# Optimization experiments

Hardware: AMD Instinct MI355X
Metric: run time of the kernel (lower is better)

Reference implementation:

```python
import jax, jax.numpy as jnp
import numpy as np

D = 1024      # d_model
H = 16        # nhead
DH = D // H   # d_head = 64
DC = D // 4   # d_compress = 256
HID = 2048    # dim_feedforward (SwiGLU hidden)
G = 2         # num_groups
EPG = 4       # experts_per_gp
E = G * EPG   # num_experts = 8
TOPK = 2
EPS = 1e-6
B, T = 2, 2048


def _rope_sincos(t, dh):
    inv_freq = 1.0 / (10000.0 ** (jnp.arange(0, dh, 2, dtype=jnp.float32) / dh))
    ang = jnp.arange(t, dtype=jnp.float32)[:, None] * inv_freq[None, :]  # [T, dh/2]
    return jnp.sin(ang), jnp.cos(ang)


def _apply_rope(x, sin, cos):
    # x: [B, H, T, DH]; sin/cos: [T, DH/2] broadcast over B,H
    x1 = x[..., ::2]
    x2 = x[..., 1::2]
    r = jnp.stack([x1 * cos - x2 * sin, x1 * sin + x2 * cos], axis=-1)
    return r.reshape(x.shape)


def _swiglu(x):
    a, b = jnp.split(x, 2, axis=-1)
    return jax.nn.silu(a) * b


def _rmsnorm(x, w):
    return x * jax.lax.rsqrt(jnp.mean(x * x, axis=-1, keepdims=True) + EPS) * w


def reference(src, Wq, Wk_c, Wv_c, Wk, Wv, Wo,
              W_shared_in, W_shared_out, W1_shared, W2_experts,
              Wg_gate, We_gate, group_bias, expert_bias, norm1_w, norm2_w):
    Bb, Tt, C = src.shape
    # ---- Latent attention (K/V compressed to d_c then re-expanded) ----
    q = (src @ Wq).reshape(Bb, Tt, H, DH).transpose(0, 2, 1, 3)
    k = ((src @ Wk_c) @ Wk).reshape(Bb, Tt, H, DH).transpose(0, 2, 1, 3)
    v = ((src @ Wv_c) @ Wv).reshape(Bb, Tt, H, DH).transpose(0, 2, 1, 3)
    sin, cos = _rope_sincos(Tt, DH)
    q = _apply_rope(q, sin, cos)
    k = _apply_rope(k, sin, cos)
    attn = jnp.einsum('bhqd,bhkd->bhqk', q, k) / np.sqrt(DH).astype(np.float32)
    attn = jax.nn.softmax(attn, axis=-1)
    sa = jnp.einsum('bhqk,bhkd->bhqd', attn, v)
    sa = sa.transpose(0, 2, 1, 3).reshape(Bb, Tt, C) @ Wo
    x = _rmsnorm(src + sa, norm1_w)

    # ---- Hierarchical MoE FFN ----
    S = Bb * Tt
    flat = x.reshape(S, C)
    shared = _swiglu(flat @ W_shared_in) @ W_shared_out          # [S, C]
    g_probs = jax.nn.softmax(flat @ Wg_gate + group_bias, -1)    # [S, G]
    g_idx = jnp.argmax(g_probs, axis=-1)                          # [S]
    e_logits = flat @ We_gate + expert_bias                       # [S, E]
    e_group = jnp.arange(E) // EPG
    in_group = e_group[None, :] == g_idx[:, None]                 # [S, E]
    e_probs = jax.nn.softmax(jnp.where(in_group, e_logits, -jnp.inf), -1)
    g_prob = jnp.take_along_axis(g_probs, g_idx[:, None], axis=1)  # [S, 1]
    p_expert = e_probs * g_prob
    topv, topi = jax.lax.top_k(p_expert, TOPK)                    # [S, K]
    # dense combine weights: zero for non-selected experts (same math as dispatch loop)
    w = jnp.zeros((S, E), flat.dtype).at[jnp.arange(S)[:, None], topi].set(topv)
    h = _swiglu(flat @ W1_shared)                                 # [S, HID] (w1 shared by all experts)
    routed = jnp.zeros_like(shared)
    for e in range(E):  # fixed small expert count
        routed = routed + (h @ W2_experts[e]) * w[:, e:e + 1]
    out = x + (shared + routed).reshape(Bb, Tt, C)
    return _rmsnorm(out, norm2_w)


def setup_inputs() -> dict:
    key = jax.random.key(0)
    ks = jax.random.split(key, 14)
    s = 0.02
    return {
        'src': jax.random.normal(ks[0], (B, T, D), jnp.float32),
        'Wq': jax.random.normal(ks[1], (D, D), jnp.float32) * s,
        'Wk_c': jax.random.normal(ks[2], (D, DC), jnp.float32) * s,
        'Wv_c': jax.random.normal(ks[3], (D, DC), jnp.float32) * s,
        'Wk': jax.random.normal(ks[4], (DC, D), jnp.float32) * s,
        'Wv': jax.random.normal(ks[5], (DC, D), jnp.float32) * s,
        'Wo': jax.random.normal(ks[6], (D, D), jnp.float32) * s,
        'W_shared_in': jax.random.normal(ks[7], (D, 2 * HID), jnp.float32) * s,
        'W_shared_out': jax.random.normal(ks[8], (HID, D), jnp.float32) * s,
        'W1_shared': jax.random.normal(ks[9], (D, 2 * HID), jnp.float32) * s,
        'W2_experts': jax.random.normal(ks[10], (E, HID, D), jnp.float32) * s,
        'Wg_gate': jax.random.normal(ks[11], (D, G), jnp.float32) * s,
        'We_gate': jax.random.normal(ks[12], (D, E), jnp.float32) * s,
        'group_bias': jnp.zeros((G,), jnp.float32),
        'expert_bias': jnp.zeros((E,), jnp.float32),
        'norm1_w': jnp.ones((D,), jnp.float32),
        'norm2_w': jnp.ones((D,), jnp.float32),
    }
```

## Files before the change

kernel.cpp:

```cpp
#include <hip/hip_runtime.h>
#include <math.h>

#define D_    1024
#define H_    16
#define DH_   64
#define DC_   256
#define HID_  2048
#define E_    8
#define B_    2
#define T_    2048
#define S_    4096
#define EPS_  1e-6f
#define QKVW_ 3072

typedef unsigned short u16;
typedef short bf16x8 __attribute__((ext_vector_type(8)));
typedef float f32x4 __attribute__((ext_vector_type(4)));

__device__ __forceinline__ float b2f(u16 u) {
    return __uint_as_float(((unsigned int)u) << 16);
}
__device__ __forceinline__ u16 f2b(float f) {
    unsigned int u = __float_as_uint(f);
    u += 0x7FFF + ((u >> 16) & 1);
    return (u16)(u >> 16);
}
__device__ __forceinline__ void g2l16(const u16* g, u16* l) {
    __builtin_amdgcn_global_load_lds(
        (const __attribute__((address_space(1))) void*)g,
        (__attribute__((address_space(3))) void*)l, 16, 0, 0);
}

__global__ __launch_bounds__(256) void conv_t(const float* __restrict__ in,
                                              u16* __restrict__ out,
                                              int K, int N,
                                              long inZ, long outZ, int perm) {
    in  += (long)blockIdx.z * inZ;
    out += (long)blockIdx.z * outZ;
    __shared__ float t[32][33];
    const int n0 = blockIdx.x * 32, k0 = blockIdx.y * 32;
    int src_n0 = n0;
    if (perm) {
        int t64 = n0 >> 6;
        src_n0 = ((n0 & 63) == 0) ? t64 * 32 : (N / 2 + t64 * 32);
    }
    const int tx = threadIdx.x & 31, ty = threadIdx.x >> 5;
#pragma unroll
    for (int i = 0; i < 4; i++)
        t[ty + 8 * i][tx] = in[(long)(k0 + ty + 8 * i) * N + src_n0 + tx];
    __syncthreads();
#pragma unroll
    for (int i = 0; i < 4; i++)
        out[(long)(n0 + ty + 8 * i) * K + k0 + tx] = f2b(t[tx][ty + 8 * i]);
}

__global__ __launch_bounds__(256) void vt_conv(const u16* __restrict__ qkv,
                                               u16* __restrict__ vt) {
    __shared__ u16 t[32][34];
    const int bh = blockIdx.z;
    const int b = bh >> 4, h = bh & 15;
    const int t0 = blockIdx.x * 32, d0 = blockIdx.y * 32;
    const int tx = threadIdx.x & 31, ty = threadIdx.x >> 5;
#pragma unroll
    for (int i = 0; i < 4; i++)
        t[ty + 8 * i][tx] =
            qkv[((long)b * T_ + t0 + ty + 8 * i) * QKVW_ + 2048 + h * 64 + d0 + tx];
    __syncthreads();
#pragma unroll
    for (int i = 0; i < 4; i++)
        vt[((long)bh * 64 + d0 + ty + 8 * i) * T_ + t0 + tx] = t[tx][ty + 8 * i];
}

__global__ __launch_bounds__(256) void convert_bf16(const float* __restrict__ in,
                                                    u16* __restrict__ out, int n4) {
    int i = blockIdx.x * 256 + threadIdx.x;
    if (i >= n4) return;
    float4 f = ((const float4*)in)[i];
    ushort4 o;
    o.x = f2b(f.x); o.y = f2b(f.y); o.z = f2b(f.z); o.w = f2b(f.w);
    ((ushort4*)out)[i] = o;
}

template<int OUTMODE>
__global__ __launch_bounds__(256) void gemm_bf16(const u16* __restrict__ A,
                                                 const u16* __restrict__ Bt,
                                                 void* __restrict__ Cp,
                                                 int N, int K, int ldo,
                                                 void* __restrict__ Cp2) {
    __shared__ u16 As[128 * 32];
    __shared__ u16 Bs[128 * 32];
    const int tid  = threadIdx.x;
    const int lane = tid & 63;
    const int wv   = tid >> 6;
    const int wm   = wv >> 1, wn = wv & 1;
    const long row0 = (long)blockIdx.y * 128;
    const long col0 = (long)blockIdx.x * 128;
    const int Klocal = K / gridDim.z;
    const long koff  = (long)blockIdx.z * Klocal;

    f32x4 acc[4][4];
#pragma unroll
    for (int i = 0; i < 4; i++)
#pragma unroll
        for (int j = 0; j < 4; j++) acc[i][j] = (f32x4){0.f, 0.f, 0.f, 0.f};

    const int sr = tid >> 2;
    const int sc = (tid & 3) << 3;
    const u16* Ag  = A  + (row0 + sr) * (long)K + koff + sc;
    const u16* Ag2 = Ag + 64 * (long)K;
    const u16* Bg  = Bt + (col0 + sr) * (long)K + koff + sc;
    const u16* Bg2 = Bg + 64 * (long)K;
    u16* lA  = As + tid * 8;
    u16* lA2 = As + 2048 + tid * 8;
    u16* lB  = Bs + tid * 8;
    u16* lB2 = Bs + 2048 + tid * 8;

    const int fl = lane & 15;
    const int fk = (lane >> 4) << 3;
    const u16* ArA = As + (wm * 64 + fl) * 32 + fk;
    const u16* BrB = Bs + (wn * 64 + fl) * 32 + fk;

    for (int k0 = 0; k0 < Klocal; k0 += 32) {
        __syncthreads();
        g2l16(Ag + k0, lA);
        g2l16(Ag2 + k0, lA2);
        g2l16(Bg + k0, lB);
        g2l16(Bg2 + k0, lB2);
        __syncthreads();
        bf16x8 af[4], bfr[4];
#pragma unroll
        for (int mi = 0; mi < 4; mi++) af[mi]  = *(const bf16x8*)(ArA + mi * 512);
#pragma unroll
        for (int ni = 0; ni < 4; ni++) bfr[ni] = *(const bf16x8*)(BrB + ni * 512);
#pragma unroll
        for (int mi = 0; mi < 4; mi++)
#pragma unroll
            for (int ni = 0; ni < 4; ni++)
                acc[mi][ni] = __builtin_amdgcn_mfma_f32_16x16x32_bf16(
                    af[mi], bfr[ni], acc[mi][ni], 0, 0, 0);
    }

    const int cr = (lane >> 4) << 2;
    const int cc = lane & 15;
#pragma unroll
    for (int mi = 0; mi < 4; mi++) {
#pragma unroll
        for (int r = 0; r < 4; r++) {
            long grow = row0 + wm * 64 + mi * 16 + cr + r;
            if (OUTMODE == 3) {
                u16* outb = (u16*)Cp + (long)(blockIdx.x >> 5) * S_ * HID_;
                u16* hrow = outb + grow * ldo + (blockIdx.x & 31) * 64 + wn * 32;
#pragma unroll
                for (int ni = 0; ni < 2; ni++) {
                    float a = acc[mi][ni][r], b = acc[mi][ni + 2][r];
                    float sig = 1.f / (1.f + __expf(-a));
                    hrow[ni * 16 + cc] = f2b(a * sig * b);
                }
            } else {
#pragma unroll
                for (int ni = 0; ni < 4; ni++) {
                    long gcol = col0 + wn * 64 + ni * 16 + cc;
                    float v = acc[mi][ni][r];
                    if (OUTMODE == 1)      ((u16*)Cp)[grow * ldo + gcol] = f2b(v);
                    else if (OUTMODE == 2) ((u16*)Cp)[gcol * ldo + grow] = f2b(v);
                    else {
                        float* basep = (float*)(blockIdx.z ? Cp2 : Cp);
                        basep[grow * ldo + gcol] = v;
                    }
                }
            }
        }
    }
}

__global__ __launch_bounds__(256) void routed_gemm(const u16* __restrict__ Hh,
                                                   const u16* __restrict__ W2T,
                                                   const int* __restrict__ list,
                                                   const float* __restrict__ wlist,
                                                   const int* __restrict__ bases,
                                                   const int* __restrict__ counts,
                                                   float* __restrict__ Cout) {
    const int e    = blockIdx.y >> 5;
    const int tile = blockIdx.y & 31;
    const int cnt  = counts[e];
    if (tile * 128 >= cnt) return;
    const int base = bases[e];

    __shared__ u16 As[128 * 32];
    __shared__ u16 Bs[128 * 32];
    __shared__ int   toks[128];
    __shared__ float wrow[128];

    const int tid = threadIdx.x;
    if (tid < 128) {
        int ridx = tile * 128 + tid;
        if (ridx < cnt) { toks[tid] = list[base + ridx]; wrow[tid] = wlist[base + ridx]; }
        else            { toks[tid] = -1;                wrow[tid] = 0.f; }
    }
    __syncthreads();

    const int lane = tid & 63;
    const int wv   = tid >> 6;
    const int wm   = wv >> 1, wn = wv & 1;
    const long col0 = (long)blockIdx.x * 128;

    f32x4 acc[4][4];
#pragma unroll
    for (int i = 0; i < 4; i++)
#pragma unroll
        for (int j = 0; j < 4; j++) acc[i][j] = (f32x4){0.f, 0.f, 0.f, 0.f};

    const int sr = tid >> 2;
    const int sc = (tid & 3) << 3;
    const int t1 = toks[sr], t2 = toks[sr + 64];
    const u16* Ag  = Hh + (long)(t1 < 0 ? 0 : t1) * HID_ + sc;
    const u16* Ag2 = Hh + (long)(t2 < 0 ? 0 : t2) * HID_ + sc;
    const u16* Bg  = W2T + (long)e * D_ * HID_ + (col0 + sr) * (long)HID_ + sc;
    const u16* Bg2 = Bg + 64 * (long)HID_;
    u16* lA  = As + tid * 8;
    u16* lA2 = As + 2048 + tid * 8;
    u16* lB  = Bs + tid * 8;
    u16* lB2 = Bs + 2048 + tid * 8;

    const int fl = lane & 15;
    const int fk = (lane >> 4) << 3;
    const u16* ArA = As + (wm * 64 + fl) * 32 + fk;
    const u16* BrB = Bs + (wn * 64 + fl) * 32 + fk;

    for (int k0 = 0; k0 < HID_; k0 += 32) {
        __syncthreads();
        g2l16(Ag + k0, lA);
        g2l16(Ag2 + k0, lA2);
        g2l16(Bg + k0, lB);
        g2l16(Bg2 + k0, lB2);
        __syncthreads();
        bf16x8 af[4], bfr[4];
#pragma unroll
        for (int mi = 0; mi < 4; mi++) af[mi]  = *(const bf16x8*)(ArA + mi * 512);
#pragma unroll
        for (int ni = 0; ni < 4; ni++) bfr[ni] = *(const bf16x8*)(BrB + ni * 512);
#pragma unroll
        for (int mi = 0; mi < 4; mi++)
#pragma unroll
            for (int ni = 0; ni < 4; ni++)
                acc[mi][ni] = __builtin_amdgcn_mfma_f32_16x16x32_bf16(
                    af[mi], bfr[ni], acc[mi][ni], 0, 0, 0);
    }

    const int cr = (lane >> 4) << 2;
    const int cc = lane & 15;
#pragma unroll
    for (int mi = 0; mi < 4; mi++) {
#pragma unroll
        for (int r = 0; r < 4; r++) {
            int rr = wm * 64 + mi * 16 + cr + r;
            int tk = toks[rr];
            if (tk < 0) continue;
            float wvw = wrow[rr];
            float* crow = Cout + (long)tk * D_ + col0 + wn * 64;
#pragma unroll
            for (int ni = 0; ni < 4; ni++)
                atomicAdd(crow + ni * 16 + cc, acc[mi][ni][r] * wvw);
        }
    }
}

__global__ __launch_bounds__(256) void rope_table(float2* __restrict__ tab) {
    int idx = blockIdx.x * 256 + threadIdx.x;
    int t = idx >> 5, i = idx & 31;
    float ang = (float)t * powf(10000.f, -(float)i / 32.f);
    float sn, cs;
    sincosf(ang, &sn, &cs);
    tab[idx] = make_float2(sn, cs);
}

__global__ __launch_bounds__(256) void rope_apply(u16* __restrict__ qkv,
                                                  const float2* __restrict__ tab) {
    long p = (long)blockIdx.x * 256 + threadIdx.x;
    int s  = (int)(p >> 8);
    int c8 = (int)(p & 255) << 3;
    int t  = s & (T_ - 1);
    const float2* tp = tab + t * 32 + ((c8 & 63) >> 1);
    u16* px = qkv + (long)s * QKVW_ + c8;
    bf16x8 v = *(const bf16x8*)px;
    bf16x8 o;
#pragma unroll
    for (int j = 0; j < 4; j++) {
        float x1 = b2f((u16)v[2 * j]), x2 = b2f((u16)v[2 * j + 1]);
        float2 sc = tp[j];
        o[2 * j]     = (short)f2b(x1 * sc.y - x2 * sc.x);
        o[2 * j + 1] = (short)f2b(x1 * sc.x + x2 * sc.y);
    }
    *(bf16x8*)px = o;
}

__global__ __launch_bounds__(512) void attn_kernel(const u16* __restrict__ qkv,
                                                   const u16* __restrict__ vtg,
                                                   u16* __restrict__ sab) {
    __shared__ u16 Ks[2][128 * 64];
    __shared__ u16 Ps[8][16 * 128];
    const int tid  = threadIdx.x;
    const int lane = tid & 63;
    const int w    = tid >> 6;
    const int flat = blockIdx.x + (blockIdx.y << 4);
    const int virt = ((flat & 7) << 6) | (flat >> 3);
    const int qt = virt & 15;
    const int bh = virt >> 4;
    const int b  = bh >> 4, h = bh & 15;
    const long tok0 = (long)b * T_ + qt * 128;
    const int fl = lane & 15;
    const int fq = lane >> 4;

    bf16x8 qf0, qf1;
    {
        const u16* qp = qkv + (tok0 + w * 16 + fl) * QKVW_ + h * 64 + fq * 8;
        qf0 = *(const bf16x8*)qp;
        qf1 = *(const bf16x8*)(qp + 32);
    }

    const u16* kb0 = qkv + ((long)b * T_) * QKVW_ + 1024 + h * 64;
    const u16* vb0 = vtg + ((long)bh * 64) * T_;

    float m_[4], l_[4];
    f32x4 oacc[4];
#pragma unroll
    for (int i = 0; i < 4; i++) {
        m_[i] = -1e30f; l_[i] = 0.f;
        oacc[i] = (f32x4){0.f, 0.f, 0.f, 0.f};
    }

    auto stageK = [&](int kt, int buf) {
#pragma unroll
        for (int ps = 0; ps < 2; ps++) {
            int i = tid + ps * 512;
            int row = i >> 3, gg = i & 7;
            g2l16(kb0 + (long)(kt * 128 + row) * QKVW_ + ((gg ^ (row & 7)) << 3),
                  Ks[buf] + i * 8);
        }
    };

    stageK(0, 0);
    int cur = 0;
    for (int kt = 0; kt < T_ / 128; kt++) {
        __syncthreads();
        if (kt + 1 < T_ / 128) stageK(kt + 1, cur ^ 1);
        const u16* kbase = Ks[cur];

        f32x4 sacc[8];
#pragma unroll
        for (int ni = 0; ni < 8; ni++) sacc[ni] = (f32x4){0.f, 0.f, 0.f, 0.f};
        __builtin_amdgcn_s_setprio(1);
#pragma unroll
        for (int ks = 0; ks < 2; ks++) {
            bf16x8 qq = ks ? qf1 : qf0;
#pragma unroll
            for (int ni = 0; ni < 8; ni++) {
                bf16x8 kf = *(const bf16x8*)(kbase + (ni * 16 + fl) * 64 +
                                             (((ks * 4 + fq) ^ (fl & 7)) << 3));
                sacc[ni] = __builtin_amdgcn_mfma_f32_16x16x32_bf16(qq, kf, sacc[ni], 0, 0, 0);
            }
        }
        __builtin_amdgcn_s_setprio(0);

        float rmax[4];
#pragma unroll
        for (int r = 0; r < 4; r++) {
            float mm = sacc[0][r];
#pragma unroll
            for (int ni = 1; ni < 8; ni++) mm = fmaxf(mm, sacc[ni][r]);
            rmax[r] = mm * 0.125f;
        }
#pragma unroll
        for (int off = 1; off < 16; off <<= 1)
#pragma unroll
            for (int r = 0; r < 4; r++) rmax[r] = fmaxf(rmax[r], __shfl_xor(rmax[r], off));
        float alpha[4], psum[4];
#pragma unroll
        for (int r = 0; r < 4; r++) {
            float nm = fmaxf(m_[r], rmax[r]);
            alpha[r] = __expf(m_[r] - nm);
            m_[r] = nm;
            psum[r] = 0.f;
        }
        u16* pst = Ps[w];
#pragma unroll
        for (int ni = 0; ni < 8; ni++) {
            int colg = ni * 2 + (fl >> 3);
            int cl   = fl & 7;
#pragma unroll
            for (int r = 0; r < 4; r++) {
                int row = fq * 4 + r;
                float p = __expf(sacc[ni][r] * 0.125f - m_[r]);
                psum[r] += p;
                pst[row * 128 + ((colg ^ (row & 15)) << 3) + cl] = f2b(p);
            }
        }
#pragma unroll
        for (int off = 1; off < 16; off <<= 1)
#pragma unroll
            for (int r = 0; r < 4; r++) psum[r] += __shfl_xor(psum[r], off);
#pragma unroll
        for (int r = 0; r < 4; r++) l_[r] = l_[r] * alpha[r] + psum[r];
#pragma unroll
        for (int ni = 0; ni < 4; ni++)
#pragma unroll
            for (int r = 0; r < 4; r++) oacc[ni][r] *= alpha[r];

        __builtin_amdgcn_s_setprio(1);
#pragma unroll
        for (int ks = 0; ks < 4; ks++) {
            bf16x8 pf = *(const bf16x8*)(pst + fl * 128 +
                                         (((ks * 4 + fq) ^ fl) << 3));
#pragma unroll
            for (int ni = 0; ni < 4; ni++) {
                const u16* vp = vb0 + (long)(ni * 16 + fl) * T_ + kt * 128 +
                                ((ks * 4 + fq) << 3);
                bf16x8 vf = *(const bf16x8*)vp;
                oacc[ni] = __builtin_amdgcn_mfma_f32_16x16x32_bf16(pf, vf, oacc[ni], 0, 0, 0);
            }
        }
        __builtin_amdgcn_s_setprio(0);
        cur ^= 1;
    }

#pragma unroll
    for (int r = 0; r < 4; r++) {
        float inv = 1.f / l_[r];
        u16* op = sab + (tok0 + w * 16 + fq * 4 + r) * D_ + h * 64 + fl;
#pragma unroll
        for (int ni = 0; ni < 4; ni++) op[ni * 16] = f2b(oacc[ni][r] * inv);
    }
}

template<int BF>
__global__ __launch_bounds__(256) void rmsnorm_res(const float* __restrict__ a,
                                                   const float* __restrict__ b,
                                                   const float* __restrict__ b2,
                                                   const float* __restrict__ w,
                                                   float* __restrict__ outf,
                                                   u16* __restrict__ outb) {
    const int s = blockIdx.x;
    const float* ar = a + (long)s * D_;
    const float* br = b + (long)s * D_;
    const float* cr2 = b2 + (long)s * D_;
    float y[4];
    float ss = 0.f;
#pragma unroll
    for (int kx = 0; kx < 4; kx++) {
        int j = threadIdx.x + kx * 256;
        y[kx] = ar[j] + br[j] + cr2[j];
        ss += y[kx] * y[kx];
    }
    __shared__ float red[4];
#pragma unroll
    for (int off = 32; off > 0; off >>= 1) ss += __shfl_down(ss, off);
    int lane = threadIdx.x & 63, wv = threadIdx.x >> 6;
    if (lane == 0) red[wv] = ss;
    __syncthreads();
    float tot = red[0] + red[1] + red[2] + red[3];
    float scl = rsqrtf(tot / (float)D_ + EPS_);
    float* orow = outf + (long)s * D_;
#pragma unroll
    for (int kx = 0; kx < 4; kx++) {
        int j = threadIdx.x + kx * 256;
        float v = y[kx] * scl * w[j];
        orow[j] = v;
        if (BF) outb[(long)s * D_ + j] = f2b(v);
    }
}

__global__ __launch_bounds__(256) void gate_kernel(const float* __restrict__ x,
                                                   const float* __restrict__ Wg,
                                                   const float* __restrict__ We,
                                                   const float* __restrict__ gb,
                                                   const float* __restrict__ eb,
                                                   int* __restrict__ tok_e,
                                                   float* __restrict__ tok_w) {
    const int wave = threadIdx.x >> 6;
    const int lane = threadIdx.x & 63;
    const int s = blockIdx.x * 4 + wave;
    const float* xr = x + (long)s * D_;
    float g0 = 0.f, g1 = 0.f;
    float ee[8];
#pragma unroll
    for (int e = 0; e < 8; e++) ee[e] = 0.f;
    for (int j = lane; j < D_; j += 64) {
        float xv = xr[j];
        g0 += xv * Wg[j * 2 + 0];
        g1 += xv * Wg[j * 2 + 1];
#pragma unroll
        for (int e = 0; e < 8; e++) ee[e] += xv * We[j * 8 + e];
    }
#pragma unroll
    for (int off = 32; off > 0; off >>= 1) {
        g0 += __shfl_down(g0, off);
        g1 += __shfl_down(g1, off);
#pragma unroll
        for (int e = 0; e < 8; e++) ee[e] += __shfl_down(ee[e], off);
    }
    if (lane == 0) {
        g0 += gb[0];
        g1 += gb[1];
        int gidx = (g1 > g0) ? 1 : 0;
        float gm = fmaxf(g0, g1);
        float p0 = expf(g0 - gm), p1 = expf(g1 - gm);
        float gprob = (gidx ? p1 : p0) / (p0 + p1);
        int base = gidx * 4;
        float pe[4];
        float em = -1e30f;
#pragma unroll
        for (int i = 0; i < 4; i++) {
            pe[i] = ee[base + i] + eb[base + i];
            em = fmaxf(em, pe[i]);
        }
        float sum = 0.f;
#pragma unroll
        for (int i = 0; i < 4; i++) { pe[i] = expf(pe[i] - em); sum += pe[i]; }
        float inv = gprob / sum;
#pragma unroll
        for (int i = 0; i < 4; i++) pe[i] *= inv;
        int i1 = 0;
        for (int i = 1; i < 4; i++) if (pe[i] > pe[i1]) i1 = i;
        int i2 = -1;
        for (int i = 0; i < 4; i++) {
            if (i == i1) continue;
            if (i2 < 0 || pe[i] > pe[i2]) i2 = i;
        }
        tok_e[s * 2 + 0] = base + i1;
        tok_e[s * 2 + 1] = base + i2;
        tok_w[s * 2 + 0] = pe[i1];
        tok_w[s * 2 + 1] = pe[i2];
    }
}

__global__ __launch_bounds__(256) void route_build(const int* __restrict__ tok_e,
                                                   const float* __restrict__ tok_w,
                                                   int* __restrict__ counts_g,
                                                   int* __restrict__ bases_g,
                                                   int* __restrict__ list,
                                                   float* __restrict__ wlist) {
    __shared__ int cnt[E_], bas[E_], cur[E_];
    const int tid = threadIdx.x;
    if (tid < E_) cnt[tid] = 0;
    __syncthreads();
    for (int i = tid; i < 2 * S_; i += 256) atomicAdd(&cnt[tok_e[i]], 1);
    __syncthreads();
    if (tid == 0) {
        int acc = 0;
        for (int e = 0; e < E_; e++) { bas[e] = acc; cur[e] = acc; acc += cnt[e]; }
    }
    __syncthreads();
    if (tid < E_) { counts_g[tid] = cnt[tid]; bases_g[tid] = bas[tid]; }
    for (int i = tid; i < 2 * S_; i += 256) {
        int e = tok_e[i];
        int p = atomicAdd(&cur[e], 1);
        list[p] = i >> 1;
        wlist[p] = tok_w[i];
    }
}

extern "C" void kernel_launch(void* const* d_in, const int* in_sizes, int n_in,
                              void* d_out, int out_size, void* d_ws, size_t ws_size,
                              hipStream_t stream) {
    const float* src  = (const float*)d_in[0];
    const float* Wq   = (const float*)d_in[1];
    const float* Wk_c = (const float*)d_in[2];
    const float* Wv_c = (const float*)d_in[3];
    const float* Wk   = (const float*)d_in[4];
    const float* Wv   = (const float*)d_in[5];
    const float* Wo   = (const float*)d_in[6];
    const float* Wsin = (const float*)d_in[7];
    const float* Wsout= (const float*)d_in[8];
    const float* W1   = (const float*)d_in[9];
    const float* W2   = (const float*)d_in[10];
    const float* Wg   = (const float*)d_in[11];
    const float* We   = (const float*)d_in[12];
    const float* gb   = (const float*)d_in[13];
    const float* eb   = (const float*)d_in[14];
    const float* n1w  = (const float*)d_in[15];
    const float* n2w  = (const float*)d_in[16];
    float* out = (float*)d_out;

    const size_t MB = 1u << 20;
    char* w8 = (char*)d_ws;
    u16*  qkv   = (u16*)(w8);
    u16*  vtg   = (u16*)(w8 + 24 * MB);
    float* oproj0 = (float*)(w8);
    float* oproj1 = (float*)(w8 + 16 * MB);
    u16*  w2t   = (u16*)(w8);
    u16*  WkcB  = (u16*)(w8 + 24 * MB);
    u16*  WvcB  = (u16*)(w8 + 24 * MB + 512 * 1024);
    u16*  WkTs  = (u16*)(w8 + 25 * MB);
    u16*  WvTs  = (u16*)(w8 + 25 * MB + 512 * 1024);
    u16*  sab   = (u16*)(w8 + 32 * MB);
    float* tokw = (float*)(w8 + 32 * MB);
    float* wlist = tokw + 2 * S_;
    int* toke   = (int*)(wlist + 2 * S_);
    int* list   = toke + 2 * S_;
    int* counts = list + 2 * S_;
    int* bases  = counts + E_;
    float* x1   = (float*)(w8 + 40 * MB);
    float* ffn0 = (float*)(w8 + 56 * MB);
    u16*  x1b   = (u16*)(w8 + 72 * MB);
    u16*  hbuf  = (u16*)(w8 + 80 * MB);
    u16*  srcb  = (u16*)(w8 + 96 * MB);
    float2* rtab= (float2*)(w8 + 104 * MB);
    u16*  hbuf2 = (u16*)(w8 + 96 * MB);
    u16*  WqkvT = (u16*)(w8 + 112 * MB);
    u16*  WsoutT= (u16*)(w8 + 112 * MB);
    u16*  WoT   = (u16*)(w8 + 118 * MB);
    u16*  WsinT = (u16*)(w8 + 120 * MB);
    u16*  W1T   = (u16*)(w8 + 128 * MB);
    float* ffn1 = (float*)(w8 + 120 * MB);

    dim3 blk(256);

    conv_t<<<dim3(32, 32), blk, 0, stream>>>(Wq, WqkvT, 1024, 1024, 0, 0, 0);
    convert_bf16<<<dim3(D_ * DC_ / 4 / 256), blk, 0, stream>>>(Wk_c, WkcB, D_ * DC_ / 4);
    convert_bf16<<<dim3(D_ * DC_ / 4 / 256), blk, 0, stream>>>(Wv_c, WvcB, D_ * DC_ / 4);
    conv_t<<<dim3(32, 8), blk, 0, stream>>>(Wk, WkTs, 256, 1024, 0, 0, 0);
    conv_t<<<dim3(32, 8), blk, 0, stream>>>(Wv, WvTs, 256, 1024, 0, 0, 0);
    gemm_bf16<2><<<dim3(8, 8), blk, 0, stream>>>(WkcB, WkTs, WqkvT + 1024 * 1024, 1024, 256, 1024, nullptr);
    gemm_bf16<2><<<dim3(8, 8), blk, 0, stream>>>(WvcB, WvTs, WqkvT + 2048 * 1024, 1024, 256, 1024, nullptr);

    convert_bf16<<<dim3(S_ * D_ / 4 / 256), blk, 0, stream>>>(src, srcb, S_ * D_ / 4);

    gemm_bf16<1><<<dim3(24, 32), blk, 0, stream>>>(srcb, WqkvT, qkv, QKVW_, 1024, QKVW_, nullptr);

    conv_t<<<dim3(32, 32), blk, 0, stream>>>(Wo, WoT, 1024, 1024, 0, 0, 0);
    conv_t<<<dim3(128, 32), blk, 0, stream>>>(Wsin, WsinT, 1024, 4096, 0, 0, 1);
    conv_t<<<dim3(32, 64), blk, 0, stream>>>(Wsout, WsoutT, 2048, 1024, 0, 0, 0);
    conv_t<<<dim3(128, 32), blk, 0, stream>>>(W1, W1T, 1024, 4096, 0, 0, 1);

    rope_table<<<dim3(T_ * 32 / 256), blk, 0, stream>>>(rtab);
    rope_apply<<<dim3(S_ * 2048 / 8 / 256), blk, 0, stream>>>(qkv, rtab);

    vt_conv<<<dim3(T_ / 32, 2, B_ * H_), blk, 0, stream>>>(qkv, vtg);
    attn_kernel<<<dim3(T_ / 128, B_ * H_), dim3(512), 0, stream>>>(qkv, vtg, sab);

    gemm_bf16<5><<<dim3(8, 32, 2), blk, 0, stream>>>(sab, WoT, oproj0, 1024, 1024, 1024, oproj1);
    rmsnorm_res<1><<<dim3(S_), blk, 0, stream>>>(src, oproj0, oproj1, n1w, x1, x1b);

    gemm_bf16<3><<<dim3(64, 32), blk, 0, stream>>>(x1b, WsinT, hbuf, 8192, 1024, 2048, nullptr);

    gemm_bf16<5><<<dim3(8, 32, 2), blk, 0, stream>>>(hbuf, WsoutT, ffn0, 1024, 2048, 1024, ffn1);

    gate_kernel<<<dim3(S_ / 4), blk, 0, stream>>>(x1, Wg, We, gb, eb, toke, tokw);
    route_build<<<dim3(1), blk, 0, stream>>>(toke, tokw, counts, bases, list, wlist);

    conv_t<<<dim3(32, 64, 8), blk, 0, stream>>>(W2, w2t, 2048, 1024,
                                                (long)HID_ * D_, (long)D_ * HID_, 0);
    routed_gemm<<<dim3(8, E_ * 32), blk, 0, stream>>>(hbuf2, w2t, list, wlist,
                                                      bases, counts, ffn0);

    rmsnorm_res<0><<<dim3(S_), blk, 0, stream>>>(x1, ffn0, ffn1, n2w, out, (u16*)nullptr);
}
```

Measured before the change: 761.3 us.

## Stage K and V through registers into LDS with lazy softmax rescale

The attention kernel now stages both K and V tiles in shared memory. It loads the next tile into registers while the current tile is computed, replacing the async double-buffered K-only staging and the direct global V reads inside the MFMA loop. It also skips the online-softmax rescaling of the output accumulators unless some row's max grows by more than a threshold. The kernel gains a minimum-occupancy launch bound. In exchange it adds an extra barrier per iteration and more register pressure from holding the prefetched tiles. The lazy rescale relies on exp(x-m) staying bounded by e^8, which is a numerical assumption.

```diff
diff --git a/kernel.cpp b/kernel.cpp
--- a/kernel.cpp
+++ b/kernel.cpp
@@ -294,10 +294,11 @@
     *(bf16x8*)px = o;
 }
 
-__global__ __launch_bounds__(512) void attn_kernel(const u16* __restrict__ qkv,
-                                                   const u16* __restrict__ vtg,
-                                                   u16* __restrict__ sab) {
-    __shared__ u16 Ks[2][128 * 64];
+__global__ __launch_bounds__(512, 4) void attn_kernel(const u16* __restrict__ qkv,
+                                                      const u16* __restrict__ vtg,
+                                                      u16* __restrict__ sab) {
+    __shared__ u16 Ks[128 * 64];
+    __shared__ u16 Vs[64 * 128];
     __shared__ u16 Ps[8][16 * 128];
     const int tid  = threadIdx.x;
     const int lane = tid & 63;
@@ -321,6 +322,35 @@
     const u16* kb0 = qkv + ((long)b * T_) * QKVW_ + 1024 + h * 64;
     const u16* vb0 = vtg + ((long)bh * 64) * T_;
 
+    const int kr0 = tid >> 3,         kgg = tid & 7;
+    const int kr1 = (tid + 512) >> 3;
+    const int vr0 = tid >> 4,         vgg = tid & 15;
+    const int vr1 = (tid + 512) >> 4;
+    const u16* kp0 = kb0 + (long)kr0 * QKVW_ + ((kgg ^ (kr0 & 7)) << 3);
+    const u16* kp1 = kb0 + (long)kr1 * QKVW_ + ((kgg ^ (kr1 & 7)) << 3);
+    const u16* vp0 = vb0 + (long)vr0 * T_ + ((vgg ^ (vr0 & 15)) << 3);
+    const u16* vp1 = vb0 + (long)vr1 * T_ + ((vgg ^ (vr1 & 15)) << 3);
+    u16* kl0 = Ks + tid * 8;
+    u16* kl1 = Ks + (tid + 512) * 8;
+    u16* vl0 = Vs + tid * 8;
+    u16* vl1 = Vs + (tid + 512) * 8;
+
+    bf16x8 kreg0, kreg1, vreg0, vreg1;
+    auto stage_load = [&](int kt) {
+        const long ko = (long)kt * 128 * QKVW_;
+        const int  vo = kt * 128;
+        kreg0 = *(const bf16x8*)(kp0 + ko);
+        kreg1 = *(const bf16x8*)(kp1 + ko);
+        vreg0 = *(const bf16x8*)(vp0 + vo);
+        vreg1 = *(const bf16x8*)(vp1 + vo);
+    };
+    auto stage_write = [&]() {
+        *(bf16x8*)kl0 = kreg0;
+        *(bf16x8*)kl1 = kreg1;
+        *(bf16x8*)vl0 = vreg0;
+        *(bf16x8*)vl1 = vreg1;
+    };
+
     float m_[4], l_[4];
     f32x4 oacc[4];
 #pragma unroll
@@ -329,22 +359,13 @@
         oacc[i] = (f32x4){0.f, 0.f, 0.f, 0.f};
     }
 
-    auto stageK = [&](int kt, int buf) {
-#pragma unroll
-        for (int ps = 0; ps < 2; ps++) {
-            int i = tid + ps * 512;
-            int row = i >> 3, gg = i & 7;
-            g2l16(kb0 + (long)(kt * 128 + row) * QKVW_ + ((gg ^ (row & 7)) << 3),
-                  Ks[buf] + i * 8);
-        }
-    };
-
-    stageK(0, 0);
-    int cur = 0;
+    stage_load(0);
+    stage_write();
+    __syncthreads();
+
     for (int kt = 0; kt < T_ / 128; kt++) {
-        __syncthreads();
-        if (kt + 1 < T_ / 128) stageK(kt + 1, cur ^ 1);
-        const u16* kbase = Ks[cur];
+        const bool pf = (kt + 1 < T_ / 128);
+        if (pf) stage_load(kt + 1);
 
         f32x4 sacc[8];
 #pragma unroll
@@ -355,7 +376,7 @@
             bf16x8 qq = ks ? qf1 : qf0;
 #pragma unroll
             for (int ni = 0; ni < 8; ni++) {
-                bf16x8 kf = *(const bf16x8*)(kbase + (ni * 16 + fl) * 64 +
+                bf16x8 kf = *(const bf16x8*)(Ks + (ni * 16 + fl) * 64 +
                                              (((ks * 4 + fq) ^ (fl & 7)) << 3));
                 sacc[ni] = __builtin_amdgcn_mfma_f32_16x16x32_bf16(qq, kf, sacc[ni], 0, 0, 0);
             }
@@ -374,14 +395,28 @@
         for (int off = 1; off < 16; off <<= 1)
 #pragma unroll
             for (int r = 0; r < 4; r++) rmax[r] = fmaxf(rmax[r], __shfl_xor(rmax[r], off));
-        float alpha[4], psum[4];
+
+        bool grow = false;
+        float nm[4];
 #pragma unroll
         for (int r = 0; r < 4; r++) {
-            float nm = fmaxf(m_[r], rmax[r]);
-            alpha[r] = __expf(m_[r] - nm);
-            m_[r] = nm;
-            psum[r] = 0.f;
-        }
+            nm[r] = fmaxf(m_[r], rmax[r]);
+            grow = grow || (rmax[r] > m_[r] + 8.f);
+        }
+        if (__any(grow)) {
+#pragma unroll
+            for (int r = 0; r < 4; r++) {
+                float a = __expf(m_[r] - nm[r]);
+                m_[r] = nm[r];
+                l_[r] *= a;
+#pragma unroll
+                for (int ni = 0; ni < 4; ni++) oacc[ni][r] *= a;
+            }
+        }
+
+        float psum[4];
+#pragma unroll
+        for (int r = 0; r < 4; r++) psum[r] = 0.f;
         u16* pst = Ps[w];
 #pragma unroll
         for (int ni = 0; ni < 8; ni++) {
@@ -400,27 +435,27 @@
 #pragma unroll
             for (int r = 0; r < 4; r++) psum[r] += __shfl_xor(psum[r], off);
 #pragma unroll
-        for (int r = 0; r < 4; r++) l_[r] = l_[r] * alpha[r] + psum[r];
-#pragma unroll
-        for (int ni = 0; ni < 4; ni++)
-#pragma unroll
-            for (int r = 0; r < 4; r++) oacc[ni][r] *= alpha[r];
+        for (int r = 0; r < 4; r++) l_[r] += psum[r];
 
         __builtin_amdgcn_s_setprio(1);
 #pragma unroll
         for (int ks = 0; ks < 4; ks++) {
-            bf16x8 pf = *(const bf16x8*)(pst + fl * 128 +
-                                         (((ks * 4 + fq) ^ fl) << 3));
+            bf16x8 pfr = *(const bf16x8*)(pst + fl * 128 +
+                                          (((ks * 4 + fq) ^ fl) << 3));
 #pragma unroll
             for (int ni = 0; ni < 4; ni++) {
-                const u16* vp = vb0 + (long)(ni * 16 + fl) * T_ + kt * 128 +
-                                ((ks * 4 + fq) << 3);
-                bf16x8 vf = *(const bf16x8*)vp;
-                oacc[ni] = __builtin_amdgcn_mfma_f32_16x16x32_bf16(pf, vf, oacc[ni], 0, 0, 0);
+                bf16x8 vf = *(const bf16x8*)(Vs + (ni * 16 + fl) * 128 +
+                                             (((ks * 4 + fq) ^ fl) << 3));
+                oacc[ni] = __builtin_amdgcn_mfma_f32_16x16x32_bf16(pfr, vf, oacc[ni], 0, 0, 0);
             }
         }
         __builtin_amdgcn_s_setprio(0);
-        cur ^= 1;
+
+        __syncthreads();
+        if (pf) {
+            stage_write();
+            __syncthreads();
+        }
     }
 
 #pragma unroll
```

Result: faster. 694.5 us (-8.8%).
